# Optimization experiments

Hardware: AMD Instinct MI355X
Metric: run time of the kernel (lower is better)

Reference implementation:

```python
import jax, jax.numpy as jnp
import numpy as np

NUM_ATOMS = 4_000_000
NUM_TYPES = 11

def setup_inputs() -> dict:
    key = jax.random.key(0)
    k1, k2 = jax.random.split(key)
    input_coords = jax.random.normal(k1, (3 * NUM_ATOMS,), dtype=jnp.float32)
    atom_types = jax.random.randint(k2, (NUM_ATOMS,), 0, NUM_TYPES, dtype=jnp.int64)
    return {"input_coords": input_coords, "atom_types": atom_types, "num_atom_types": NUM_TYPES}

def reference(input_coords, atom_types, num_atom_types):
    # counts per atom type  [T]
    counts = jnp.bincount(atom_types, length=num_atom_types).astype(jnp.int32)
    # exclusive prefix sum -> bucket offsets  [T]
    offsets = (jnp.cumsum(counts) - counts).astype(jnp.int32)
    # stable sort by type reproduces the C++ bucket fill order:
    # atoms of the same type keep their original relative order.
    perm = jnp.argsort(atom_types, stable=True)  # [N] source index for each output slot
    coords3 = input_coords.reshape(-1, 3)        # [N,3]
    typed_coords = coords3[perm].reshape(-1)     # [3N] type-grouped flat coords
    return typed_coords, counts, offsets
```

## Files before the change

### kernel.cpp

```cpp
#include <hip/hip_runtime.h>

#define NTYPES 11
#define BLOCK  256
#define ITEMS  8
#define CHUNK  (BLOCK * ITEMS)
#define MAXCH  32

__global__ __launch_bounds__(BLOCK) void hist_kernel(
    const int* __restrict__ types, int N, int B, int* __restrict__ bc) {
  __shared__ int shCnt[NTYPES];
  const int tid = threadIdx.x;
  const int b = blockIdx.x;
  if (tid < NTYPES) shCnt[tid] = 0;
  __syncthreads();

  const int run = b * CHUNK + tid * ITEMS;
  int cnt[NTYPES];
#pragma unroll
  for (int t = 0; t < NTYPES; ++t) cnt[t] = 0;

  if (run < N) {
    const int4* p = (const int4*)(types + run);
    int4 a0 = p[0], a1 = p[1];
    int ty[ITEMS] = {a0.x, a0.y, a0.z, a0.w, a1.x, a1.y, a1.z, a1.w};
#pragma unroll
    for (int k = 0; k < ITEMS; ++k) {
#pragma unroll
      for (int t = 0; t < NTYPES; ++t) cnt[t] += (ty[k] == t) ? 1 : 0;
    }
  }

  const int lane = tid & 63;
#pragma unroll
  for (int t = 0; t < NTYPES; ++t) {
    int v = cnt[t];
    for (int o = 32; o >= 1; o >>= 1) v += __shfl_down(v, o);
    if (lane == 0) atomicAdd(&shCnt[t], v);
  }
  __syncthreads();
  if (tid < NTYPES) bc[tid * B + b] = shCnt[tid];
}

__global__ __launch_bounds__(NTYPES * 64) void scan_kernel(
    const int* __restrict__ bc, int B, int* __restrict__ scanOut,
    int* __restrict__ offs, float* __restrict__ outTail) {
  __shared__ int totals[NTYPES];
  const int lane = threadIdx.x & 63;
  const int t = threadIdx.x >> 6;
  const int nch = (B + 63) >> 6;

  int x[MAXCH];
#pragma unroll
  for (int c = 0; c < MAXCH; ++c) {
    const int idx = c * 64 + lane;
    x[c] = (c < nch && idx < B) ? bc[t * B + idx] : 0;
  }

  int carry = 0;
#pragma unroll
  for (int c = 0; c < MAXCH; ++c) {
    if (c >= nch) break;
    int incl = x[c];
#pragma unroll
    for (int o = 1; o < 64; o <<= 1) {
      int v = __shfl_up(incl, o);
      if (lane >= o) incl += v;
    }
    incl += carry;
    const int idx = c * 64 + lane;
    if (idx < B) scanOut[t * B + idx] = incl - x[c];
    carry = __shfl(incl, 63);
  }
  if (lane == 0) totals[t] = carry;
  __syncthreads();

  if (threadIdx.x == 0) {
    int off = 0;
    for (int u = 0; u < NTYPES; ++u) {
      const int c = totals[u];
      offs[u] = off;
      outTail[u] = (float)c;
      outTail[NTYPES + u] = (float)off;
      off += c;
    }
  }
}

__global__ __launch_bounds__(BLOCK) void scatter_kernel(
    const float* __restrict__ coords, const int* __restrict__ types,
    const int* __restrict__ scanOut, const int* __restrict__ offs, int N,
    int B, float* __restrict__ out) {
  __shared__ float shC[CHUNK * 3];
  __shared__ int wtot[NTYPES][4];
  __shared__ int shOff[NTYPES + 1];
  __shared__ int shDelta[NTYPES];

  const int tid = threadIdx.x;
  const int b = blockIdx.x;
  const int lane = tid & 63;
  const int wave = tid >> 6;
  const int run = b * CHUNK + tid * ITEMS;
  const bool active = (run < N);

  int ty[ITEMS];
  int cnt[NTYPES];
#pragma unroll
  for (int t = 0; t < NTYPES; ++t) cnt[t] = 0;
#pragma unroll
  for (int k = 0; k < ITEMS; ++k) ty[k] = -1;

  float c[ITEMS * 3];
  if (active) {
    const int4* p = (const int4*)(types + run);
    int4 a0 = p[0], a1 = p[1];
    int tt[ITEMS] = {a0.x, a0.y, a0.z, a0.w, a1.x, a1.y, a1.z, a1.w};
#pragma unroll
    for (int k = 0; k < ITEMS; ++k) ty[k] = tt[k];
    const float4* cp = (const float4*)(coords + (size_t)run * 3);
#pragma unroll
    for (int q = 0; q < (ITEMS * 3) / 4; ++q) {
      float4 v = cp[q];
      c[4 * q + 0] = v.x;
      c[4 * q + 1] = v.y;
      c[4 * q + 2] = v.z;
      c[4 * q + 3] = v.w;
    }
#pragma unroll
    for (int k = 0; k < ITEMS; ++k) {
#pragma unroll
      for (int t = 0; t < NTYPES; ++t) cnt[t] += (ty[k] == t) ? 1 : 0;
    }
  }

  int rank[NTYPES];
#pragma unroll
  for (int t = 0; t < NTYPES; ++t) {
    int incl = cnt[t];
#pragma unroll
    for (int o = 1; o < 64; o <<= 1) {
      int v = __shfl_up(incl, o);
      if (lane >= o) incl += v;
    }
    if (lane == 63) wtot[t][wave] = incl;
    rank[t] = incl - cnt[t];
  }
  __syncthreads();

  if (tid < NTYPES) {
    int loc = 0;
    for (int u = 0; u < tid; ++u)
      loc += wtot[u][0] + wtot[u][1] + wtot[u][2] + wtot[u][3];
    shOff[tid] = loc;
    shDelta[tid] = 3 * (offs[tid] + scanOut[tid * B + b] - loc);
    if (tid == NTYPES - 1) {
      shOff[NTYPES] =
          loc + wtot[tid][0] + wtot[tid][1] + wtot[tid][2] + wtot[tid][3];
    }
  }
  __syncthreads();

#pragma unroll
  for (int t = 0; t < NTYPES; ++t) {
    int wb = 0;
#pragma unroll
    for (int w = 0; w < 3; ++w) wb += (w < wave) ? wtot[t][w] : 0;
    rank[t] += wb + shOff[t];
  }

  if (active) {
#pragma unroll
    for (int k = 0; k < ITEMS; ++k) {
      const int t0 = ty[k];
      int slot = 0;
#pragma unroll
      for (int t = 0; t < NTYPES; ++t) {
        if (t0 == t) {
          slot = rank[t];
          rank[t] += 1;
        }
      }
      shC[3 * slot + 0] = c[3 * k + 0];
      shC[3 * slot + 1] = c[3 * k + 1];
      shC[3 * slot + 2] = c[3 * k + 2];
    }
  }
  __syncthreads();

  const int total = shOff[NTYPES];
  int offr[NTYPES];
  int dlt[NTYPES];
#pragma unroll
  for (int t = 0; t < NTYPES; ++t) {
    offr[t] = shOff[t];
    dlt[t] = shDelta[t];
  }
#pragma unroll
  for (int k = 0; k < ITEMS; ++k) {
    const int s = k * BLOCK + tid;
    if (s < total) {
      int d = dlt[0];
#pragma unroll
      for (int t = 1; t < NTYPES; ++t) d = (s >= offr[t]) ? dlt[t] : d;
      const int src = 3 * s;
      out[src + d + 0] = shC[src + 0];
      out[src + d + 1] = shC[src + 1];
      out[src + d + 2] = shC[src + 2];
    }
  }
}

extern "C" void kernel_launch(void* const* d_in, const int* in_sizes, int n_in,
                              void* d_out, int out_size, void* d_ws,
                              size_t ws_size, hipStream_t stream) {
  const float* coords = (const float*)d_in[0];
  const int* types = (const int*)d_in[1];
  const int N = in_sizes[1];
  const int B = (N + CHUNK - 1) / CHUNK;

  int* bc = (int*)d_ws;
  int* scanOut = bc + NTYPES * B;
  int* offs = scanOut + NTYPES * B;
  float* out = (float*)d_out;
  float* outTail = out + (size_t)3 * N;

  hist_kernel<<<B, BLOCK, 0, stream>>>(types, N, B, bc);
  scan_kernel<<<1, NTYPES * 64, 0, stream>>>(bc, B, scanOut, offs, outTail);
  scatter_kernel<<<B, BLOCK, 0, stream>>>(coords, types, scanOut, offs, N, B,
                                          out);
}
```

Before: 134.0 us.

## Move per-block ranking into histogram pass and store compact slot metadata

```diff
diff --git a/kernel.cpp b/kernel.cpp
--- a/kernel.cpp
+++ b/kernel.cpp
@@ -7,94 +7,10 @@
 #define MAXCH  32
 
 __global__ __launch_bounds__(BLOCK) void hist_kernel(
-    const int* __restrict__ types, int N, int B, int* __restrict__ bc) {
-  __shared__ int shCnt[NTYPES];
-  const int tid = threadIdx.x;
-  const int b = blockIdx.x;
-  if (tid < NTYPES) shCnt[tid] = 0;
-  __syncthreads();
-
-  const int run = b * CHUNK + tid * ITEMS;
-  int cnt[NTYPES];
-#pragma unroll
-  for (int t = 0; t < NTYPES; ++t) cnt[t] = 0;
-
-  if (run < N) {
-    const int4* p = (const int4*)(types + run);
-    int4 a0 = p[0], a1 = p[1];
-    int ty[ITEMS] = {a0.x, a0.y, a0.z, a0.w, a1.x, a1.y, a1.z, a1.w};
-#pragma unroll
-    for (int k = 0; k < ITEMS; ++k) {
-#pragma unroll
-      for (int t = 0; t < NTYPES; ++t) cnt[t] += (ty[k] == t) ? 1 : 0;
-    }
-  }
-
-  const int lane = tid & 63;
-#pragma unroll
-  for (int t = 0; t < NTYPES; ++t) {
-    int v = cnt[t];
-    for (int o = 32; o >= 1; o >>= 1) v += __shfl_down(v, o);
-    if (lane == 0) atomicAdd(&shCnt[t], v);
-  }
-  __syncthreads();
-  if (tid < NTYPES) bc[tid * B + b] = shCnt[tid];
-}
-
-__global__ __launch_bounds__(NTYPES * 64) void scan_kernel(
-    const int* __restrict__ bc, int B, int* __restrict__ scanOut,
-    int* __restrict__ offs, float* __restrict__ outTail) {
-  __shared__ int totals[NTYPES];
-  const int lane = threadIdx.x & 63;
-  const int t = threadIdx.x >> 6;
-  const int nch = (B + 63) >> 6;
-
-  int x[MAXCH];
-#pragma unroll
-  for (int c = 0; c < MAXCH; ++c) {
-    const int idx = c * 64 + lane;
-    x[c] = (c < nch && idx < B) ? bc[t * B + idx] : 0;
-  }
-
-  int carry = 0;
-#pragma unroll
-  for (int c = 0; c < MAXCH; ++c) {
-    if (c >= nch) break;
-    int incl = x[c];
-#pragma unroll
-    for (int o = 1; o < 64; o <<= 1) {
-      int v = __shfl_up(incl, o);
-      if (lane >= o) incl += v;
-    }
-    incl += carry;
-    const int idx = c * 64 + lane;
-    if (idx < B) scanOut[t * B + idx] = incl - x[c];
-    carry = __shfl(incl, 63);
-  }
-  if (lane == 0) totals[t] = carry;
-  __syncthreads();
-
-  if (threadIdx.x == 0) {
-    int off = 0;
-    for (int u = 0; u < NTYPES; ++u) {
-      const int c = totals[u];
-      offs[u] = off;
-      outTail[u] = (float)c;
-      outTail[NTYPES + u] = (float)off;
-      off += c;
-    }
-  }
-}
-
-__global__ __launch_bounds__(BLOCK) void scatter_kernel(
-    const float* __restrict__ coords, const int* __restrict__ types,
-    const int* __restrict__ scanOut, const int* __restrict__ offs, int N,
-    int B, float* __restrict__ out) {
-  __shared__ float shC[CHUNK * 3];
+    const int* __restrict__ types, int N, int B, int* __restrict__ bc,
+    unsigned short* __restrict__ meta) {
   __shared__ int wtot[NTYPES][4];
-  __shared__ int shOff[NTYPES + 1];
-  __shared__ int shDelta[NTYPES];
-
+  __shared__ int shOff[NTYPES];
   const int tid = threadIdx.x;
   const int b = blockIdx.x;
   const int lane = tid & 63;
@@ -109,13 +25,176 @@
 #pragma unroll
   for (int k = 0; k < ITEMS; ++k) ty[k] = -1;
 
-  float c[ITEMS * 3];
   if (active) {
     const int4* p = (const int4*)(types + run);
     int4 a0 = p[0], a1 = p[1];
     int tt[ITEMS] = {a0.x, a0.y, a0.z, a0.w, a1.x, a1.y, a1.z, a1.w};
 #pragma unroll
     for (int k = 0; k < ITEMS; ++k) ty[k] = tt[k];
+#pragma unroll
+    for (int k = 0; k < ITEMS; ++k) {
+#pragma unroll
+      for (int t = 0; t < NTYPES; ++t) cnt[t] += (ty[k] == t) ? 1 : 0;
+    }
+  }
+
+  int rank[NTYPES];
+#pragma unroll
+  for (int t = 0; t < NTYPES; ++t) {
+    int incl = cnt[t];
+#pragma unroll
+    for (int o = 1; o < 64; o <<= 1) {
+      int v = __shfl_up(incl, o);
+      if (lane >= o) incl += v;
+    }
+    if (lane == 63) wtot[t][wave] = incl;
+    rank[t] = incl - cnt[t];
+  }
+  __syncthreads();
+
+  if (tid < NTYPES) {
+    int loc = 0;
+    for (int u = 0; u < tid; ++u)
+      loc += wtot[u][0] + wtot[u][1] + wtot[u][2] + wtot[u][3];
+    shOff[tid] = loc;
+    bc[tid * B + b] =
+        wtot[tid][0] + wtot[tid][1] + wtot[tid][2] + wtot[tid][3];
+  }
+  __syncthreads();
+
+#pragma unroll
+  for (int t = 0; t < NTYPES; ++t) {
+    int wb = 0;
+#pragma unroll
+    for (int w = 0; w < 3; ++w) wb += (w < wave) ? wtot[t][w] : 0;
+    rank[t] += wb + shOff[t];
+  }
+
+  if (active) {
+    unsigned int m[ITEMS];
+#pragma unroll
+    for (int k = 0; k < ITEMS; ++k) {
+      const int t0 = ty[k];
+      int slot = 0;
+#pragma unroll
+      for (int t = 0; t < NTYPES; ++t) {
+        if (t0 == t) {
+          slot = rank[t];
+          rank[t] += 1;
+        }
+      }
+      m[k] = (unsigned int)(slot | (t0 << 11));
+    }
+    int4 mv;
+    mv.x = (int)(m[0] | (m[1] << 16));
+    mv.y = (int)(m[2] | (m[3] << 16));
+    mv.z = (int)(m[4] | (m[5] << 16));
+    mv.w = (int)(m[6] | (m[7] << 16));
+    *(int4*)(meta + run) = mv;
+  }
+}
+
+__global__ __launch_bounds__(NTYPES * 64) void scan_kernel(
+    const int* __restrict__ bc, int B, int* __restrict__ gBase,
+    float* __restrict__ outTail) {
+  __shared__ int totals[NTYPES];
+  __shared__ int offsSh[NTYPES];
+  const int lane = threadIdx.x & 63;
+  const int t = threadIdx.x >> 6;
+  const int nch = (B + 63) >> 6;
+
+  int x[MAXCH], ex[MAXCH];
+#pragma unroll
+  for (int c = 0; c < MAXCH; ++c) {
+    const int idx = c * 64 + lane;
+    x[c] = (c < nch && idx < B) ? bc[t * B + idx] : 0;
+  }
+
+  int carry = 0;
+#pragma unroll
+  for (int c = 0; c < MAXCH; ++c) {
+    if (c >= nch) break;
+    int incl = x[c];
+#pragma unroll
+    for (int o = 1; o < 64; o <<= 1) {
+      int v = __shfl_up(incl, o);
+      if (lane >= o) incl += v;
+    }
+    ex[c] = carry + incl - x[c];
+    carry += __shfl(incl, 63);
+  }
+  if (lane == 0) totals[t] = carry;
+  __syncthreads();
+
+  if (threadIdx.x == 0) {
+    int off = 0;
+    for (int u = 0; u < NTYPES; ++u) {
+      const int c = totals[u];
+      offsSh[u] = off;
+      outTail[u] = (float)c;
+      outTail[NTYPES + u] = (float)off;
+      off += c;
+    }
+  }
+  __syncthreads();
+
+  const int offt = offsSh[t];
+#pragma unroll
+  for (int c = 0; c < MAXCH; ++c) {
+    if (c >= nch) break;
+    const int idx = c * 64 + lane;
+    if (idx < B) gBase[t * B + idx] = ex[c] + offt;
+  }
+}
+
+__global__ __launch_bounds__(BLOCK) void scatter_kernel(
+    const float* __restrict__ coords, const unsigned short* __restrict__ meta,
+    const int* __restrict__ bc, const int* __restrict__ gBase, int N, int B,
+    float* __restrict__ out) {
+  __shared__ float shC[CHUNK * 3];
+  __shared__ int shOffA[NTYPES + 1];
+  __shared__ int shDelta[NTYPES];
+
+  const int tid = threadIdx.x;
+  const int b = blockIdx.x;
+  const int lane = tid & 63;
+  const int wave = tid >> 6;
+  const int run = b * CHUNK + tid * ITEMS;
+  const bool active = (run < N);
+
+  if (wave == 0) {
+    int ct = 0, gt = 0;
+    if (lane < NTYPES) {
+      ct = bc[lane * B + b];
+      gt = gBase[lane * B + b];
+    }
+    int incl = ct;
+#pragma unroll
+    for (int o = 1; o < 16; o <<= 1) {
+      int v = __shfl_up(incl, o);
+      if (lane >= o) incl += v;
+    }
+    const int excl = incl - ct;
+    if (lane < NTYPES) {
+      shOffA[lane] = excl;
+      shDelta[lane] = 3 * (gt - excl);
+    }
+    if (lane == NTYPES - 1) shOffA[NTYPES] = incl;
+  }
+
+  if (active) {
+    const int4 mv = *(const int4*)(meta + run);
+    int slot[ITEMS];
+    slot[0] = mv.x & 0x7FF;
+    slot[1] = (mv.x >> 16) & 0x7FF;
+    slot[2] = mv.y & 0x7FF;
+    slot[3] = (mv.y >> 16) & 0x7FF;
+    slot[4] = mv.z & 0x7FF;
+    slot[5] = (mv.z >> 16) & 0x7FF;
+    slot[6] = mv.w & 0x7FF;
+    slot[7] = (mv.w >> 16) & 0x7FF;
+
+    float c[ITEMS * 3];
     const float4* cp = (const float4*)(coords + (size_t)run * 3);
 #pragma unroll
     for (int q = 0; q < (ITEMS * 3) / 4; ++q) {
@@ -127,71 +206,19 @@
     }
 #pragma unroll
     for (int k = 0; k < ITEMS; ++k) {
-#pragma unroll
-      for (int t = 0; t < NTYPES; ++t) cnt[t] += (ty[k] == t) ? 1 : 0;
-    }
-  }
-
-  int rank[NTYPES];
-#pragma unroll
-  for (int t = 0; t < NTYPES; ++t) {
-    int incl = cnt[t];
-#pragma unroll
-    for (int o = 1; o < 64; o <<= 1) {
-      int v = __shfl_up(incl, o);
-      if (lane >= o) incl += v;
-    }
-    if (lane == 63) wtot[t][wave] = incl;
-    rank[t] = incl - cnt[t];
-  }
-  __syncthreads();
-
-  if (tid < NTYPES) {
-    int loc = 0;
-    for (int u = 0; u < tid; ++u)
-      loc += wtot[u][0] + wtot[u][1] + wtot[u][2] + wtot[u][3];
-    shOff[tid] = loc;
-    shDelta[tid] = 3 * (offs[tid] + scanOut[tid * B + b] - loc);
-    if (tid == NTYPES - 1) {
-      shOff[NTYPES] =
-          loc + wtot[tid][0] + wtot[tid][1] + wtot[tid][2] + wtot[tid][3];
-    }
-  }
-  __syncthreads();
-
-#pragma unroll
-  for (int t = 0; t < NTYPES; ++t) {
-    int wb = 0;
-#pragma unroll
-    for (int w = 0; w < 3; ++w) wb += (w < wave) ? wtot[t][w] : 0;
-    rank[t] += wb + shOff[t];
-  }
-
-  if (active) {
-#pragma unroll
-    for (int k = 0; k < ITEMS; ++k) {
-      const int t0 = ty[k];
-      int slot = 0;
-#pragma unroll
-      for (int t = 0; t < NTYPES; ++t) {
-        if (t0 == t) {
-          slot = rank[t];
-          rank[t] += 1;
-        }
-      }
-      shC[3 * slot + 0] = c[3 * k + 0];
-      shC[3 * slot + 1] = c[3 * k + 1];
-      shC[3 * slot + 2] = c[3 * k + 2];
-    }
-  }
-  __syncthreads();
-
-  const int total = shOff[NTYPES];
+      shC[3 * slot[k] + 0] = c[3 * k + 0];
+      shC[3 * slot[k] + 1] = c[3 * k + 1];
+      shC[3 * slot[k] + 2] = c[3 * k + 2];
+    }
+  }
+  __syncthreads();
+
+  const int total = shOffA[NTYPES];
   int offr[NTYPES];
   int dlt[NTYPES];
 #pragma unroll
   for (int t = 0; t < NTYPES; ++t) {
-    offr[t] = shOff[t];
+    offr[t] = shOffA[t];
     dlt[t] = shDelta[t];
   }
 #pragma unroll
@@ -217,14 +244,14 @@
   const int N = in_sizes[1];
   const int B = (N + CHUNK - 1) / CHUNK;
 
+  const int bcElems = ((NTYPES * B + 63) / 64) * 64;
   int* bc = (int*)d_ws;
-  int* scanOut = bc + NTYPES * B;
-  int* offs = scanOut + NTYPES * B;
+  int* gBase = bc + bcElems;
+  unsigned short* meta = (unsigned short*)(gBase + bcElems);
   float* out = (float*)d_out;
   float* outTail = out + (size_t)3 * N;
 
-  hist_kernel<<<B, BLOCK, 0, stream>>>(types, N, B, bc);
-  scan_kernel<<<1, NTYPES * 64, 0, stream>>>(bc, B, scanOut, offs, outTail);
-  scatter_kernel<<<B, BLOCK, 0, stream>>>(coords, types, scanOut, offs, N, B,
-                                          out);
-}
+  hist_kernel<<<B, BLOCK, 0, stream>>>(types, N, B, bc, meta);
+  scan_kernel<<<1, NTYPES * 64, 0, stream>>>(bc, B, gBase, outTail);
+  scatter_kernel<<<B, BLOCK, 0, stream>>>(coords, meta, bc, gBase, N, B, out);
+}
```

Result: slower. 137.5 us (+2.6%).

## Fuse block-count scan into scatter kernel, removing the single-block scan launch

Applied to the files above, without the earlier changes.

```diff
diff --git a/kernel.cpp b/kernel.cpp
--- a/kernel.cpp
+++ b/kernel.cpp
@@ -4,7 +4,6 @@
 #define BLOCK  256
 #define ITEMS  8
 #define CHUNK  (BLOCK * ITEMS)
-#define MAXCH  32
 
 __global__ __launch_bounds__(BLOCK) void hist_kernel(
     const int* __restrict__ types, int N, int B, int* __restrict__ bc) {
@@ -41,59 +40,16 @@
   if (tid < NTYPES) bc[tid * B + b] = shCnt[tid];
 }
 
-__global__ __launch_bounds__(NTYPES * 64) void scan_kernel(
-    const int* __restrict__ bc, int B, int* __restrict__ scanOut,
-    int* __restrict__ offs, float* __restrict__ outTail) {
-  __shared__ int totals[NTYPES];
-  const int lane = threadIdx.x & 63;
-  const int t = threadIdx.x >> 6;
-  const int nch = (B + 63) >> 6;
-
-  int x[MAXCH];
-#pragma unroll
-  for (int c = 0; c < MAXCH; ++c) {
-    const int idx = c * 64 + lane;
-    x[c] = (c < nch && idx < B) ? bc[t * B + idx] : 0;
-  }
-
-  int carry = 0;
-#pragma unroll
-  for (int c = 0; c < MAXCH; ++c) {
-    if (c >= nch) break;
-    int incl = x[c];
-#pragma unroll
-    for (int o = 1; o < 64; o <<= 1) {
-      int v = __shfl_up(incl, o);
-      if (lane >= o) incl += v;
-    }
-    incl += carry;
-    const int idx = c * 64 + lane;
-    if (idx < B) scanOut[t * B + idx] = incl - x[c];
-    carry = __shfl(incl, 63);
-  }
-  if (lane == 0) totals[t] = carry;
-  __syncthreads();
-
-  if (threadIdx.x == 0) {
-    int off = 0;
-    for (int u = 0; u < NTYPES; ++u) {
-      const int c = totals[u];
-      offs[u] = off;
-      outTail[u] = (float)c;
-      outTail[NTYPES + u] = (float)off;
-      off += c;
-    }
-  }
-}
-
 __global__ __launch_bounds__(BLOCK) void scatter_kernel(
     const float* __restrict__ coords, const int* __restrict__ types,
-    const int* __restrict__ scanOut, const int* __restrict__ offs, int N,
-    int B, float* __restrict__ out) {
+    const int* __restrict__ bc, int N, int B, float* __restrict__ out,
+    float* __restrict__ outTail) {
   __shared__ float shC[CHUNK * 3];
   __shared__ int wtot[NTYPES][4];
   __shared__ int shOff[NTYPES + 1];
   __shared__ int shDelta[NTYPES];
+  __shared__ int shTot[NTYPES];
+  __shared__ int shPre[NTYPES];
 
   const int tid = threadIdx.x;
   const int b = blockIdx.x;
@@ -102,6 +58,26 @@
   const int run = b * CHUNK + tid * ITEMS;
   const bool active = (run < N);
 
+  for (int t = wave; t < NTYPES; t += 4) {
+    const int* bt = bc + t * B;
+    int tot = 0, pre = 0;
+    for (int base = 0; base < B; base += 64) {
+      const int idx = base + lane;
+      const int v = (idx < B) ? bt[idx] : 0;
+      tot += v;
+      pre += (idx < b) ? v : 0;
+    }
+#pragma unroll
+    for (int m = 32; m >= 1; m >>= 1) {
+      tot += __shfl_xor(tot, m);
+      pre += __shfl_xor(pre, m);
+    }
+    if (lane == 0) {
+      shTot[t] = tot;
+      shPre[t] = pre;
+    }
+  }
+
   int ty[ITEMS];
   int cnt[NTYPES];
 #pragma unroll
@@ -109,13 +85,63 @@
 #pragma unroll
   for (int k = 0; k < ITEMS; ++k) ty[k] = -1;
 
-  float c[ITEMS * 3];
   if (active) {
     const int4* p = (const int4*)(types + run);
     int4 a0 = p[0], a1 = p[1];
     int tt[ITEMS] = {a0.x, a0.y, a0.z, a0.w, a1.x, a1.y, a1.z, a1.w};
 #pragma unroll
     for (int k = 0; k < ITEMS; ++k) ty[k] = tt[k];
+#pragma unroll
+    for (int k = 0; k < ITEMS; ++k) {
+#pragma unroll
+      for (int t = 0; t < NTYPES; ++t) cnt[t] += (ty[k] == t) ? 1 : 0;
+    }
+  }
+
+  int rank[NTYPES];
+#pragma unroll
+  for (int t = 0; t < NTYPES; ++t) {
+    int incl = cnt[t];
+#pragma unroll
+    for (int o = 1; o < 64; o <<= 1) {
+      int v = __shfl_up(incl, o);
+      if (lane >= o) incl += v;
+    }
+    if (lane == 63) wtot[t][wave] = incl;
+    rank[t] = incl - cnt[t];
+  }
+  __syncthreads();
+
+  if (tid < NTYPES) {
+    int loc = 0;
+    for (int u = 0; u < tid; ++u)
+      loc += wtot[u][0] + wtot[u][1] + wtot[u][2] + wtot[u][3];
+    shOff[tid] = loc;
+    int off = 0;
+    for (int u = 0; u < tid; ++u) off += shTot[u];
+    const int gb = off + shPre[tid];
+    shDelta[tid] = 3 * (gb - loc);
+    if (tid == NTYPES - 1) {
+      shOff[NTYPES] =
+          loc + wtot[tid][0] + wtot[tid][1] + wtot[tid][2] + wtot[tid][3];
+    }
+    if (b == 0) {
+      outTail[tid] = (float)shTot[tid];
+      outTail[NTYPES + tid] = (float)off;
+    }
+  }
+  __syncthreads();
+
+#pragma unroll
+  for (int t = 0; t < NTYPES; ++t) {
+    int wb = 0;
+#pragma unroll
+    for (int w = 0; w < 3; ++w) wb += (w < wave) ? wtot[t][w] : 0;
+    rank[t] += wb + shOff[t];
+  }
+
+  if (active) {
+    float c[ITEMS * 3];
     const float4* cp = (const float4*)(coords + (size_t)run * 3);
 #pragma unroll
     for (int q = 0; q < (ITEMS * 3) / 4; ++q) {
@@ -125,49 +151,6 @@
       c[4 * q + 2] = v.z;
       c[4 * q + 3] = v.w;
     }
-#pragma unroll
-    for (int k = 0; k < ITEMS; ++k) {
-#pragma unroll
-      for (int t = 0; t < NTYPES; ++t) cnt[t] += (ty[k] == t) ? 1 : 0;
-    }
-  }
-
-  int rank[NTYPES];
-#pragma unroll
-  for (int t = 0; t < NTYPES; ++t) {
-    int incl = cnt[t];
-#pragma unroll
-    for (int o = 1; o < 64; o <<= 1) {
-      int v = __shfl_up(incl, o);
-      if (lane >= o) incl += v;
-    }
-    if (lane == 63) wtot[t][wave] = incl;
-    rank[t] = incl - cnt[t];
-  }
-  __syncthreads();
-
-  if (tid < NTYPES) {
-    int loc = 0;
-    for (int u = 0; u < tid; ++u)
-      loc += wtot[u][0] + wtot[u][1] + wtot[u][2] + wtot[u][3];
-    shOff[tid] = loc;
-    shDelta[tid] = 3 * (offs[tid] + scanOut[tid * B + b] - loc);
-    if (tid == NTYPES - 1) {
-      shOff[NTYPES] =
-          loc + wtot[tid][0] + wtot[tid][1] + wtot[tid][2] + wtot[tid][3];
-    }
-  }
-  __syncthreads();
-
-#pragma unroll
-  for (int t = 0; t < NTYPES; ++t) {
-    int wb = 0;
-#pragma unroll
-    for (int w = 0; w < 3; ++w) wb += (w < wave) ? wtot[t][w] : 0;
-    rank[t] += wb + shOff[t];
-  }
-
-  if (active) {
 #pragma unroll
     for (int k = 0; k < ITEMS; ++k) {
       const int t0 = ty[k];
@@ -218,13 +201,10 @@
   const int B = (N + CHUNK - 1) / CHUNK;
 
   int* bc = (int*)d_ws;
-  int* scanOut = bc + NTYPES * B;
-  int* offs = scanOut + NTYPES * B;
   float* out = (float*)d_out;
   float* outTail = out + (size_t)3 * N;
 
   hist_kernel<<<B, BLOCK, 0, stream>>>(types, N, B, bc);
-  scan_kernel<<<1, NTYPES * 64, 0, stream>>>(bc, B, scanOut, offs, outTail);
-  scatter_kernel<<<B, BLOCK, 0, stream>>>(coords, types, scanOut, offs, N, B,
-                                          out);
+  scatter_kernel<<<B, BLOCK, 0, stream>>>(coords, types, bc, N, B, out,
+                                          outTail);
 }
```

Result: slower. 181.7 us (+35.7%).
